# Kernel optimization log

Hardware: AMD Instinct MI355X
Metric: run time of the kernel (lower is better)

The kernel has to match this reference:

```python
import jax, jax.numpy as jnp
import numpy as np

B, N, E, A, H, F, HEADS = 2, 16384, 262144, 3, 128, 16, 4
DH = H // HEADS
CONST = (2.0 * np.pi) ** 0.5


def setup_inputs() -> dict:
    key = jax.random.key(0)
    ks = jax.random.split(key, 16)
    s = 0.05
    return {
        "x": jax.random.normal(ks[0], (B, N, H), jnp.float32),
        "edge_index": jax.random.randint(ks[1], (2, E), 0, N),
        # per-action message MLPs (self.mlp)
        "mlp_W1": jax.random.normal(ks[2], (A, H, H), jnp.float32) * s,
        "mlp_b1": jnp.zeros((A, H), jnp.float32),
        "mlp_W2": jax.random.normal(ks[3], (A, H, H), jnp.float32) * s,
        "mlp_b2": jnp.zeros((A, H), jnp.float32),
        # transformer (MMTs) projections, 4 heads over the action axis
        "Wq": jax.random.normal(ks[4], (H, H), jnp.float32) * s,
        "bq": jnp.zeros((H,), jnp.float32),
        "Wk": jax.random.normal(ks[5], (H, H), jnp.float32) * s,
        "bk": jnp.zeros((H,), jnp.float32),
        "Wv": jax.random.normal(ks[6], (H, H), jnp.float32) * s,
        "bv": jnp.zeros((H,), jnp.float32),
        "Wo": jax.random.normal(ks[7], (H, H), jnp.float32) * s,
        "bo": jnp.zeros((H,), jnp.float32),
        # decide_mu MLPs (decide_In_sigma is never used in the original forward)
        "mu_W1": jax.random.normal(ks[8], (A, H, H), jnp.float32) * s,
        "mu_b1": jnp.zeros((A, H), jnp.float32),
        "mu_W2": jax.random.normal(ks[9], (A, H, F), jnp.float32) * s,
        "mu_b2": jnp.zeros((A, F), jnp.float32),
    }


def _forward(x, edge_index, mlp_W1, mlp_b1, mlp_W2, mlp_b2,
             Wq, bq, Wk, bk, Wv, bv, Wo, bo, mu_W1, mu_b1, mu_W2, mu_b2):
    # per-action MLP stack: (B,N,H) -> (B,N,A,H)
    h = jax.nn.relu(jnp.einsum('bnh,ahk->bnak', x, mlp_W1) + mlp_b1)
    h = jnp.einsum('bnak,akh->bnah', h, mlp_W2) + mlp_b2
    # gather along source nodes, scatter-add into destination bins
    dst, src = edge_index[0], edge_index[1]
    g = h[:, src]                                   # (B,E,A,H) ~ 800 MB
    agg = jax.ops.segment_sum(jnp.moveaxis(g, 1, 0), dst, num_segments=N)
    agg = jnp.moveaxis(agg, 0, 1)                   # (B,N,A,H)
    # multi-head self-attention over the action axis (len A) per node
    q = (jnp.einsum('bnah,hk->bnak', agg, Wq) + bq).reshape(B, N, A, HEADS, DH)
    k = (jnp.einsum('bnah,hk->bnak', agg, Wk) + bk).reshape(B, N, A, HEADS, DH)
    v = (jnp.einsum('bnah,hk->bnak', agg, Wv) + bv).reshape(B, N, A, HEADS, DH)
    scores = jnp.einsum('bnqed,bnked->bneqk', q, k) / (DH ** 0.5)
    attn = jax.nn.softmax(scores, axis=-1)
    o = jnp.einsum('bneqk,bnked->bnqed', attn, v).reshape(B, N, A, H)
    h_I = agg + jnp.einsum('bnah,hk->bnak', o, Wo) + bo  # residual
    # per-action decode to action means: (B,N,A,F)
    m = jax.nn.relu(jnp.einsum('bnah,ahk->bnak', h_I, mu_W1) + mu_b1)
    mu = jnp.einsum('bnak,akf->bnaf', m, mu_W2) + mu_b2
    # Gaussian reparameterized sampling, VAR is a non-trainable all-ones buffer
    VAR = jnp.ones((N, A, F), jnp.float32)
    noise = jax.random.normal(jax.random.key(42), mu.shape, mu.dtype)
    sample = mu + noise * VAR
    logp = -jnp.log(CONST * VAR) - (sample - mu) ** 2 / (2.0 * VAR ** 2)
    a0 = jax.nn.softmax(jnp.tanh(sample[:, :, 0, :]), axis=-1)
    a1 = jax.nn.sigmoid(sample[:, :, 1, :])
    a2 = jnp.tanh(sample[:, :, 2, :])
    sample_out = jnp.stack([a0, a1, a2], axis=2)    # (B,N,A,F)
    return sample_out, logp.sum((-1, -2))           # ((B,N,A,F),(B,N))


def reference(x, edge_index, mlp_W1, mlp_b1, mlp_W2, mlp_b2,
              Wq, bq, Wk, bk, Wv, bv, Wo, bo, mu_W1, mu_b1, mu_W2, mu_b2):
    return _forward(x, edge_index, mlp_W1, mlp_b1, mlp_W2, mlp_b2,
                    Wq, bq, Wk, bk, Wv, bv, Wo, bo, mu_W1, mu_b1, mu_W2, mu_b2)
```

## Files before the change

### kernel.cpp

```cpp
#include <hip/hip_runtime.h>

#define NN    16384
#define EE    262144
#define BNODES 32768
#define AH    384
#define TOT_NOISE 1572864u

typedef __attribute__((ext_vector_type(8))) short short8;
typedef __attribute__((ext_vector_type(4))) float v4f;

__device__ __forceinline__ unsigned short f2bf(float f) {
  unsigned u = __float_as_uint(f);
  unsigned r = u + 0x7fffu + ((u >> 16) & 1u);
  return (unsigned short)(r >> 16);
}
__device__ __forceinline__ float bf2f(unsigned short h) {
  return __uint_as_float(((unsigned)h) << 16);
}
__device__ __forceinline__ float bflo(unsigned u) { return __uint_as_float(u << 16); }
__device__ __forceinline__ float bfhi(unsigned u) { return __uint_as_float(u & 0xffff0000u); }

__device__ __forceinline__ void threefry2x32_042(unsigned& x0, unsigned& x1) {
  const unsigned ks0 = 0u;
  const unsigned ks1 = 42u;
  const unsigned ks2 = 0x1BD11BDAu ^ 0u ^ 42u;
  x0 += ks0; x1 += ks1;
#define TFR(r) { x0 += x1; x1 = (x1 << (r)) | (x1 >> (32 - (r))); x1 ^= x0; }
  TFR(13) TFR(15) TFR(26) TFR(6)   x0 += ks1; x1 += ks2 + 1u;
  TFR(17) TFR(29) TFR(16) TFR(24)  x0 += ks2; x1 += ks0 + 2u;
  TFR(13) TFR(15) TFR(26) TFR(6)   x0 += ks0; x1 += ks1 + 3u;
  TFR(17) TFR(29) TFR(16) TFR(24)  x0 += ks1; x1 += ks2 + 4u;
  TFR(13) TFR(15) TFR(26) TFR(6)   x0 += ks2; x1 += ks0 + 5u;
#undef TFR
}

__device__ __forceinline__ float erfinv_f32(float x) {
  float w = -log1pf(-x * x);
  float p;
  if (w < 5.0f) {
    w -= 2.5f;
    p = 2.81022636e-08f;
    p = fmaf(p, w, 3.43273939e-07f);
    p = fmaf(p, w, -3.5233877e-06f);
    p = fmaf(p, w, -4.39150654e-06f);
    p = fmaf(p, w, 0.00021858087f);
    p = fmaf(p, w, -0.00125372503f);
    p = fmaf(p, w, -0.00417768164f);
    p = fmaf(p, w, 0.246640727f);
    p = fmaf(p, w, 1.50140941f);
  } else {
    w = sqrtf(w) - 3.0f;
    p = -0.000200214257f;
    p = fmaf(p, w, 0.000100950558f);
    p = fmaf(p, w, 0.00134934322f);
    p = fmaf(p, w, -0.00367342844f);
    p = fmaf(p, w, 0.00573950773f);
    p = fmaf(p, w, -0.0076224613f);
    p = fmaf(p, w, 0.00943887047f);
    p = fmaf(p, w, 1.00167406f);
    p = fmaf(p, w, 2.83297682f);
  }
  return p * x;
}

__device__ __forceinline__ unsigned jax_random_bits32(unsigned i) {
  unsigned x0 = 0u, x1 = i;
  threefry2x32_042(x0, x1);
  return x0 ^ x1;
}

__device__ __forceinline__ float jax_normal_from_bits(unsigned bits) {
  float f = __uint_as_float((bits >> 9) | 0x3f800000u) - 1.0f;
  const float lo = -0.99999994f;
  float u = f * 2.0f + lo;
  u = fmaxf(u, lo);
  return 1.4142135623730951f * erfinv_f32(u);
}

__global__ void edge_count(const int* __restrict__ dst, int* __restrict__ deg) {
  int e = blockIdx.x * 256 + threadIdx.x;
  if (e < EE) atomicAdd(&deg[dst[e]], 1);
}

__global__ __launch_bounds__(256) void scan_k(const int* __restrict__ deg,
                                              int* __restrict__ offs,
                                              int* __restrict__ cur) {
  __shared__ int part[256];
  int t = threadIdx.x;
  int base = t * 64;
  int s = 0;
  for (int i = 0; i < 64; i++) s += deg[base + i];
  part[t] = s;
  __syncthreads();
  for (int off = 1; off < 256; off <<= 1) {
    int v = (t >= off) ? part[t - off] : 0;
    __syncthreads();
    part[t] += v;
    __syncthreads();
  }
  int run = (t == 0) ? 0 : part[t - 1];
  for (int i = 0; i < 64; i++) {
    offs[base + i] = run;
    cur[base + i] = run;
    run += deg[base + i];
  }
  if (t == 255) offs[NN] = run;
}

__global__ void edge_fill(const int* __restrict__ dst, const int* __restrict__ srcv,
                          int* __restrict__ cur, int* __restrict__ csr) {
  int e = blockIdx.x * 256 + threadIdx.x;
  if (e < EE) {
    int d = dst[e];
    int p = atomicAdd(&cur[d], 1);
    csr[p] = srcv[e];
  }
}

__global__ __launch_bounds__(256) void prep_wfrag(
    const float* __restrict__ W1, const float* __restrict__ W2,
    const float* __restrict__ mW1,
    const float* __restrict__ Wq, const float* __restrict__ Wk,
    const float* __restrict__ Wv, const float* __restrict__ Wo,
    unsigned short* __restrict__ F) {
  int m = blockIdx.y;
  const float* W;
  if (m < 3) W = W1 + (long)m * 16384;
  else if (m < 6) W = W2 + (long)(m - 3) * 16384;
  else if (m < 9) W = mW1 + (long)(m - 6) * 16384;
  else W = (m == 9) ? Wq : (m == 10) ? Wk : (m == 11) ? Wv : Wo;
  int f = blockIdx.x * 256 + threadIdx.x;
  int tile = f >> 9;
  int kt = tile >> 3, nt = tile & 7;
  int r = f & 511;
  int lane = r >> 3, j = r & 7;
  int k = kt * 32 + (lane >> 4) * 8 + j;
  int n = nt * 16 + (lane & 15);
  F[(long)m * 16384 + f] = f2bf(W[k * 128 + n]);
}

__global__ __launch_bounds__(256) void prep_w2frag(
    const float* __restrict__ mW2, unsigned short* __restrict__ F2) {
  int a = blockIdx.y;
  int f = blockIdx.x * 256 + threadIdx.x;
  int kt = f >> 9;
  int r = f & 511;
  int lane = r >> 3, j = r & 7;
  int k = kt * 32 + (lane >> 4) * 8 + j;
  int n = lane & 15;
  F2[a * 2048 + f] = f2bf(mW2[(a * 128 + k) * 16 + n]);
}

#define GXSTR 136
__global__ __launch_bounds__(256) void gemm_bf16(
    const unsigned short* __restrict__ X, long xRowStride, long xAOff,
    const unsigned short* __restrict__ WF,
    const float* __restrict__ Bias, long bAStride,
    unsigned short* __restrict__ C, long cRowStride, long cAOff,
    int relu, int xfp32) {
  __shared__ __align__(16) unsigned short As[128 * GXSTR];
  const int a = blockIdx.y;
  const long m0 = (long)blockIdx.x * 128;
  const int tid = threadIdx.x;
  const unsigned short* Wp = WF + (long)a * 16384;

  if (xfp32) {
    const float* Xf = (const float*)X + (long)a * xAOff + m0 * xRowStride;
#pragma unroll
    for (int p = 0; p < 8; p++) {
      int c = tid + p * 256;
      int row = c >> 4, c8 = (c & 15) * 8;
      float4 v1 = *(const float4*)(Xf + (long)row * xRowStride + c8);
      float4 v2 = *(const float4*)(Xf + (long)row * xRowStride + c8 + 4);
      short8 o;
      o[0] = (short)f2bf(v1.x); o[1] = (short)f2bf(v1.y);
      o[2] = (short)f2bf(v1.z); o[3] = (short)f2bf(v1.w);
      o[4] = (short)f2bf(v2.x); o[5] = (short)f2bf(v2.y);
      o[6] = (short)f2bf(v2.z); o[7] = (short)f2bf(v2.w);
      *(short8*)(&As[row * GXSTR + c8]) = o;
    }
  } else {
    const unsigned short* Xp = X + (long)a * xAOff + m0 * xRowStride;
#pragma unroll
    for (int p = 0; p < 8; p++) {
      int c = tid + p * 256;
      int row = c >> 4, c8 = (c & 15) * 8;
      short8 v = *(const short8*)(Xp + (long)row * xRowStride + c8);
      *(short8*)(&As[row * GXSTR + c8]) = v;
    }
  }
  __syncthreads();

  const int w = tid >> 6;
  const int l = tid & 63;
  const int lr = l & 15;
  const int lg = l >> 4;

  v4f acc[8][2];
#pragma unroll
  for (int mt = 0; mt < 8; mt++) {
    acc[mt][0] = (v4f){0.f, 0.f, 0.f, 0.f};
    acc[mt][1] = (v4f){0.f, 0.f, 0.f, 0.f};
  }

#pragma unroll
  for (int kt = 0; kt < 4; kt++) {
    short8 bfr[2];
#pragma unroll
    for (int ntl = 0; ntl < 2; ntl++)
      bfr[ntl] = *(const short8*)(Wp + (long)(kt * 8 + 2 * w + ntl) * 512 + l * 8);
#pragma unroll
    for (int mt = 0; mt < 8; mt++) {
      short8 af = *(const short8*)(&As[(mt * 16 + lr) * GXSTR + kt * 32 + lg * 8]);
      acc[mt][0] = __builtin_amdgcn_mfma_f32_16x16x32_bf16(af, bfr[0], acc[mt][0], 0, 0, 0);
      acc[mt][1] = __builtin_amdgcn_mfma_f32_16x16x32_bf16(af, bfr[1], acc[mt][1], 0, 0, 0);
    }
  }

  float bv[2] = {Bias[(long)a * bAStride + 32 * w + lr],
                 Bias[(long)a * bAStride + 32 * w + 16 + lr]};
#pragma unroll
  for (int mt = 0; mt < 8; mt++)
#pragma unroll
    for (int ntl = 0; ntl < 2; ntl++)
#pragma unroll
      for (int i = 0; i < 4; i++) {
        long row = m0 + mt * 16 + lg * 4 + i;
        int col = 32 * w + ntl * 16 + lr;
        float t = acc[mt][ntl][i] + bv[ntl];
        if (relu) t = fmaxf(t, 0.0f);
        C[row * cRowStride + (long)a * cAOff + col] = f2bf(t);
      }
}

__global__ __launch_bounds__(192) void aggregate_bf2(
    const unsigned short* __restrict__ H, const int* __restrict__ offs,
    const int* __restrict__ csr, unsigned short* __restrict__ AGB) {
  const int n = blockIdx.x;
  const int t = threadIdx.x;
  const int bt = t / 96;
  const int c = (t % 96) * 4;
  const int e0 = offs[n], e1 = offs[n + 1];
  const unsigned short* hb = H + (long)bt * NN * 384 + c;
  float a0 = 0.f, a1 = 0.f, a2 = 0.f, a3 = 0.f;
  int j = e0;
  for (; j + 4 <= e1; j += 4) {
    int s0 = csr[j], s1 = csr[j + 1], s2 = csr[j + 2], s3 = csr[j + 3];
    uint2 u0 = *(const uint2*)(hb + (long)s0 * 384);
    uint2 u1 = *(const uint2*)(hb + (long)s1 * 384);
    uint2 u2 = *(const uint2*)(hb + (long)s2 * 384);
    uint2 u3 = *(const uint2*)(hb + (long)s3 * 384);
    a0 += bflo(u0.x); a1 += bfhi(u0.x); a2 += bflo(u0.y); a3 += bfhi(u0.y);
    a0 += bflo(u1.x); a1 += bfhi(u1.x); a2 += bflo(u1.y); a3 += bfhi(u1.y);
    a0 += bflo(u2.x); a1 += bfhi(u2.x); a2 += bflo(u2.y); a3 += bfhi(u2.y);
    a0 += bflo(u3.x); a1 += bfhi(u3.x); a2 += bflo(u3.y); a3 += bfhi(u3.y);
  }
  for (; j < e1; j++) {
    int s = csr[j];
    uint2 u = *(const uint2*)(hb + (long)s * 384);
    a0 += bflo(u.x); a1 += bfhi(u.x); a2 += bflo(u.y); a3 += bfhi(u.y);
  }
  uint2 out;
  out.x = (unsigned)f2bf(a0) | ((unsigned)f2bf(a1) << 16);
  out.y = (unsigned)f2bf(a2) | ((unsigned)f2bf(a3) << 16);
  *(uint2*)(AGB + ((long)bt * NN + n) * 384 + c) = out;
}

#define XSTR 136
#define QSTR 34
__global__ __launch_bounds__(256, 3) void attn_mfma(
    const unsigned short* __restrict__ AGB, const unsigned short* __restrict__ WF,
    const float* __restrict__ bq, const float* __restrict__ bk,
    const float* __restrict__ bv, const float* __restrict__ bo,
    unsigned short* __restrict__ OUTB) {
  __shared__ __align__(16) unsigned short xS[48 * XSTR];
  __shared__ __align__(16) unsigned short qS[4 * 48 * QSTR];
  __shared__ __align__(16) unsigned short kS[4 * 48 * QSTR];
  __shared__ __align__(16) unsigned short vS[4 * 48 * QSTR];

  const int tid = threadIdx.x;
  const long node0 = (long)blockIdx.x * 16;
  const unsigned short* src = AGB + node0 * 384;

#pragma unroll
  for (int p = 0; p < 3; p++) {
    int c = tid + p * 256;
    int row = c >> 4, c8 = (c & 15) * 8;
    short8 v = *(const short8*)(src + c * 8);
    *(short8*)(&xS[row * XSTR + c8]) = v;
  }
  __syncthreads();

  const int w = tid >> 6;
  const int l = tid & 63;
  const int lr = l & 15;
  const int lg = l >> 4;
  const unsigned short* WQ = WF;
  const unsigned short* WK = WF + 16384;
  const unsigned short* WV = WF + 32768;
  const unsigned short* WO = WF + 49152;

  v4f accq[3][2], acck[3][2], accv[3][2];
#pragma unroll
  for (int mt = 0; mt < 3; mt++)
#pragma unroll
    for (int n = 0; n < 2; n++) {
      accq[mt][n] = (v4f){0.f, 0.f, 0.f, 0.f};
      acck[mt][n] = (v4f){0.f, 0.f, 0.f, 0.f};
      accv[mt][n] = (v4f){0.f, 0.f, 0.f, 0.f};
    }

#pragma unroll
  for (int kt = 0; kt < 4; kt++) {
    short8 af[3];
#pragma unroll
    for (int mt = 0; mt < 3; mt++)
      af[mt] = *(const short8*)&xS[(mt * 16 + lr) * XSTR + kt * 32 + lg * 8];
#pragma unroll
    for (int ntl = 0; ntl < 2; ntl++) {
      long tf = (long)(kt * 8 + 2 * w + ntl) * 512 + l * 8;
      short8 b0 = *(const short8*)&WQ[tf];
      short8 b1 = *(const short8*)&WK[tf];
      short8 b2 = *(const short8*)&WV[tf];
#pragma unroll
      for (int mt = 0; mt < 3; mt++) {
        accq[mt][ntl] = __builtin_amdgcn_mfma_f32_16x16x32_bf16(af[mt], b0, accq[mt][ntl], 0, 0, 0);
        acck[mt][ntl] = __builtin_amdgcn_mfma_f32_16x16x32_bf16(af[mt], b1, acck[mt][ntl], 0, 0, 0);
        accv[mt][ntl] = __builtin_amdgcn_mfma_f32_16x16x32_bf16(af[mt], b2, accv[mt][ntl], 0, 0, 0);
      }
    }
  }

  {
    const float scale = 0.17677669529663687f;
    unsigned short* qw = &qS[w * 48 * QSTR];
    unsigned short* kw = &kS[w * 48 * QSTR];
    unsigned short* vw = &vS[w * 48 * QSTR];
    float bqv[2] = {bq[32 * w + lr], bq[32 * w + 16 + lr]};
    float bkv[2] = {bk[32 * w + lr], bk[32 * w + 16 + lr]};
    float bvv[2] = {bv[32 * w + lr], bv[32 * w + 16 + lr]};
#pragma unroll
    for (int mt = 0; mt < 3; mt++)
#pragma unroll
      for (int ntl = 0; ntl < 2; ntl++)
#pragma unroll
        for (int i = 0; i < 4; i++) {
          int row = mt * 16 + lg * 4 + i;
          int col = ntl * 16 + lr;
          qw[row * QSTR + col] = f2bf((accq[mt][ntl][i] + bqv[ntl]) * scale);
          kw[row * QSTR + col] = f2bf(acck[mt][ntl][i] + bkv[ntl]);
          vw[row * QSTR + col] = f2bf(accv[mt][ntl][i] + bvv[ntl]);
        }
  }

  float resv[3][2][4];
#pragma unroll
  for (int mt = 0; mt < 3; mt++)
#pragma unroll
    for (int ntl = 0; ntl < 2; ntl++)
#pragma unroll
      for (int i = 0; i < 4; i++)
        resv[mt][ntl][i] =
            bf2f(xS[(mt * 16 + lg * 4 + i) * XSTR + 32 * w + ntl * 16 + lr]);
  __syncthreads();

  if (l < 48) {
    int aq = l % 3;
    int ndr = l - aq;
    const unsigned* qr = (const unsigned*)&qS[(w * 48 + l) * QSTR];
    const unsigned* kr0 = (const unsigned*)&kS[(w * 48 + ndr) * QSTR];
    const unsigned* kr1 = (const unsigned*)&kS[(w * 48 + ndr + 1) * QSTR];
    const unsigned* kr2 = (const unsigned*)&kS[(w * 48 + ndr + 2) * QSTR];
    float s0 = 0.f, s1 = 0.f, s2 = 0.f;
#pragma unroll
    for (int j = 0; j < 16; j++) {
      unsigned uq = qr[j], u0 = kr0[j], u1 = kr1[j], u2 = kr2[j];
      float qa = bflo(uq), qb = bfhi(uq);
      s0 = fmaf(qa, bflo(u0), fmaf(qb, bfhi(u0), s0));
      s1 = fmaf(qa, bflo(u1), fmaf(qb, bfhi(u1), s1));
      s2 = fmaf(qa, bflo(u2), fmaf(qb, bfhi(u2), s2));
    }
    float mx = fmaxf(s0, fmaxf(s1, s2));
    float e0 = expf(s0 - mx), e1 = expf(s1 - mx), e2 = expf(s2 - mx);
    float inv = 1.0f / (e0 + e1 + e2);
    e0 *= inv; e1 *= inv; e2 *= inv;
    const unsigned* vr0 = (const unsigned*)&vS[(w * 48 + ndr) * QSTR];
    const unsigned* vr1 = (const unsigned*)&vS[(w * 48 + ndr + 1) * QSTR];
    const unsigned* vr2 = (const unsigned*)&vS[(w * 48 + ndr + 2) * QSTR];
    unsigned ov[16];
#pragma unroll
    for (int j = 0; j < 16; j++) {
      unsigned u0 = vr0[j], u1 = vr1[j], u2 = vr2[j];
      float oa = fmaf(e0, bflo(u0), fmaf(e1, bflo(u1), e2 * bflo(u2)));
      float ob = fmaf(e0, bfhi(u0), fmaf(e1, bfhi(u1), e2 * bfhi(u2)));
      ov[j] = (unsigned)f2bf(oa) | ((unsigned)f2bf(ob) << 16);
    }
    uint4* orow = (uint4*)&xS[l * XSTR + 32 * w];
    orow[0] = make_uint4(ov[0], ov[1], ov[2], ov[3]);
    orow[1] = make_uint4(ov[4], ov[5], ov[6], ov[7]);
    orow[2] = make_uint4(ov[8], ov[9], ov[10], ov[11]);
    orow[3] = make_uint4(ov[12], ov[13], ov[14], ov[15]);
  }
  __syncthreads();

  v4f acco[3][2];
#pragma unroll
  for (int mt = 0; mt < 3; mt++)
#pragma unroll
    for (int n = 0; n < 2; n++) acco[mt][n] = (v4f){0.f, 0.f, 0.f, 0.f};

#pragma unroll
  for (int kt = 0; kt < 4; kt++) {
    short8 af[3];
#pragma unroll
    for (int mt = 0; mt < 3; mt++)
      af[mt] = *(const short8*)&xS[(mt * 16 + lr) * XSTR + kt * 32 + lg * 8];
#pragma unroll
    for (int ntl = 0; ntl < 2; ntl++) {
      long tf = (long)(kt * 8 + 2 * w + ntl) * 512 + l * 8;
      short8 b = *(const short8*)&WO[tf];
#pragma unroll
      for (int mt = 0; mt < 3; mt++)
        acco[mt][ntl] = __builtin_amdgcn_mfma_f32_16x16x32_bf16(af[mt], b, acco[mt][ntl], 0, 0, 0);
    }
  }

  {
    float bov[2] = {bo[32 * w + lr], bo[32 * w + 16 + lr]};
#pragma unroll
    for (int mt = 0; mt < 3; mt++)
#pragma unroll
      for (int ntl = 0; ntl < 2; ntl++)
#pragma unroll
        for (int i = 0; i < 4; i++) {
          int row = mt * 16 + lg * 4 + i;
          int gcol = 32 * w + ntl * 16 + lr;
          OUTB[(node0 * 3 + row) * 128 + gcol] =
              f2bf(acco[mt][ntl][i] + bov[ntl] + resv[mt][ntl][i]);
        }
  }
}

#define MSTR 136
__global__ __launch_bounds__(256) void mu_final(
    const unsigned short* __restrict__ M, const unsigned short* __restrict__ WF2,
    const float* __restrict__ mb2,
    float* __restrict__ out0, float* __restrict__ out1) {
  __shared__ __align__(16) unsigned short As[192 * MSTR];
  __shared__ float lpS[192];
  const int tid = threadIdx.x;
  const long bn0 = (long)blockIdx.x * 64;

#pragma unroll
  for (int p = 0; p < 12; p++) {
    int ch = tid + p * 256;
    int nd = ch / 48;
    int rest = ch % 48;
    int a = rest >> 4;
    int k8 = (rest & 15) * 8;
    short8 v = *(const short8*)(M + (bn0 + nd) * 384 + a * 128 + k8);
    *(short8*)(&As[(a * 64 + nd) * MSTR + k8]) = v;
  }
  __syncthreads();

  const int w = tid >> 6, l = tid & 63, lr = l & 15, lg = l >> 4;

  v4f acc[3];
#pragma unroll
  for (int t = 0; t < 3; t++) acc[t] = (v4f){0.f, 0.f, 0.f, 0.f};

#pragma unroll
  for (int kt = 0; kt < 4; kt++) {
#pragma unroll
    for (int t = 0; t < 3; t++) {
      int tile = 3 * w + t;
      int a = tile >> 2;
      short8 af = *(const short8*)(&As[(tile * 16 + lr) * MSTR + kt * 32 + lg * 8]);
      short8 bf = *(const short8*)(WF2 + a * 2048 + kt * 512 + l * 8);
      acc[t] = __builtin_amdgcn_mfma_f32_16x16x32_bf16(af, bf, acc[t], 0, 0, 0);
    }
  }

#pragma unroll
  for (int t = 0; t < 3; t++) {
    int tile = 3 * w + t;
    int a = tile >> 2;
    int ndbase = (tile & 3) * 16;
    float bias = mb2[a * 16 + lr];
#pragma unroll
    for (int i = 0; i < 4; i++) {
      int nd = ndbase + lg * 4 + i;
      float mu = acc[t][i] + bias;
      unsigned gidx = (unsigned)((bn0 + nd) * 48 + a * 16 + lr);
      unsigned bits = jax_random_bits32(gidx);
      float noise = jax_normal_from_bits(bits);
      float sample = mu + noise;
      float lp = -0.9189385332046727f - 0.5f * noise * noise;
      lp += __shfl_xor(lp, 1, 64);
      lp += __shfl_xor(lp, 2, 64);
      lp += __shfl_xor(lp, 4, 64);
      lp += __shfl_xor(lp, 8, 64);
      if (lr == 0) lpS[a * 64 + nd] = lp;
      float res;
      if (a == 0) {
        float th = tanhf(sample);
        float mx = th;
        mx = fmaxf(mx, __shfl_xor(mx, 1, 64));
        mx = fmaxf(mx, __shfl_xor(mx, 2, 64));
        mx = fmaxf(mx, __shfl_xor(mx, 4, 64));
        mx = fmaxf(mx, __shfl_xor(mx, 8, 64));
        float ex = expf(th - mx);
        float ss = ex;
        ss += __shfl_xor(ss, 1, 64);
        ss += __shfl_xor(ss, 2, 64);
        ss += __shfl_xor(ss, 4, 64);
        ss += __shfl_xor(ss, 8, 64);
        res = ex / ss;
      } else if (a == 1) {
        res = 1.0f / (1.0f + expf(-sample));
      } else {
        res = tanhf(sample);
      }
      out0[gidx] = res;
    }
  }
  __syncthreads();
  if (tid < 64)
    out1[bn0 + tid] = lpS[tid] + lpS[64 + tid] + lpS[128 + tid];
}

extern "C" void kernel_launch(void* const* d_in, const int* in_sizes, int n_in,
                              void* d_out, int out_size, void* d_ws, size_t ws_size,
                              hipStream_t stream) {
  const float* x = (const float*)d_in[0];
  const int* ei = (const int*)d_in[1];
  const float* W1 = (const float*)d_in[2];
  const float* b1 = (const float*)d_in[3];
  const float* W2 = (const float*)d_in[4];
  const float* b2 = (const float*)d_in[5];
  const float* Wq = (const float*)d_in[6];
  const float* bq = (const float*)d_in[7];
  const float* Wk = (const float*)d_in[8];
  const float* bk = (const float*)d_in[9];
  const float* Wv = (const float*)d_in[10];
  const float* bv = (const float*)d_in[11];
  const float* Wo = (const float*)d_in[12];
  const float* bo = (const float*)d_in[13];
  const float* mW1 = (const float*)d_in[14];
  const float* mb1 = (const float*)d_in[15];
  const float* mW2 = (const float*)d_in[16];
  const float* mb2 = (const float*)d_in[17];
  (void)in_sizes; (void)n_in; (void)out_size; (void)ws_size;

  unsigned short* T1 = (unsigned short*)d_ws;
  unsigned short* HB = T1 + 12582912;
  unsigned short* AGB = HB + 12582912;
  int* deg = (int*)(AGB + 12582912);
  int* offs = deg + NN;
  int* cur = offs + (NN + 1);
  int* csr = cur + NN;
  unsigned short* wfrag = (unsigned short*)(((uintptr_t)(csr + EE) + 15) & ~(uintptr_t)15);
  unsigned short* w2frag = wfrag + 13 * 16384;

  const int* dst = ei;
  const int* srcv = ei + EE;

  float* out0 = (float*)d_out;
  float* out1 = out0 + TOT_NOISE;

  hipMemsetAsync(deg, 0, NN * sizeof(int), stream);
  edge_count<<<EE / 256, 256, 0, stream>>>(dst, deg);
  scan_k<<<1, 256, 0, stream>>>(deg, offs, cur);
  edge_fill<<<EE / 256, 256, 0, stream>>>(dst, srcv, cur, csr);
  prep_wfrag<<<dim3(64, 13), 256, 0, stream>>>(W1, W2, mW1, Wq, Wk, Wv, Wo, wfrag);
  prep_w2frag<<<dim3(8, 3), 256, 0, stream>>>(mW2, w2frag);

  dim3 g128(BNODES / 128, 3);
  gemm_bf16<<<g128, 256, 0, stream>>>((const unsigned short*)x, 128, 0, wfrag, b1, 128, T1, AH, 128, 1, 1);
  gemm_bf16<<<g128, 256, 0, stream>>>(T1, AH, 128, wfrag + 3 * 16384, b2, 128, HB, AH, 128, 0, 0);
  aggregate_bf2<<<NN, 192, 0, stream>>>(HB, offs, csr, AGB);
  attn_mfma<<<BNODES / 16, 256, 0, stream>>>(AGB, wfrag + 9 * 16384, bq, bk, bv, bo, T1);
  gemm_bf16<<<g128, 256, 0, stream>>>(T1, AH, 128, wfrag + 6 * 16384, mb1, 128, HB, AH, 128, 1, 0);
  mu_final<<<BNODES / 64, 256, 0, stream>>>(HB, w2frag, mb2, out0, out1);
}
```

Measured before the change: 277.3 us.

## Fuse MLP GEMMs, merge decode into attention, restructure aggregation with prefetch

The two per-action MLP GEMMs become one kernel that keeps the intermediate activation in shared memory instead of writing and rereading it from global memory. The mu decode MLP and the sampling epilogue move into the attention kernel, so the attention output no longer round-trips through global memory and two launches disappear. The aggregation kernel now maps each block to two nodes of one batch and prefetches CSR indices in groups of eight. The attention kernel becomes longer and heavier on registers, and the aggregation now reads each CSR range once per batch instead of sharing it across both batches in one block.

```diff
diff --git a/kernel.cpp b/kernel.cpp
--- a/kernel.cpp
+++ b/kernel.cpp
@@ -152,49 +152,34 @@
 }
 
 #define GXSTR 136
-__global__ __launch_bounds__(256) void gemm_bf16(
-    const unsigned short* __restrict__ X, long xRowStride, long xAOff,
-    const unsigned short* __restrict__ WF,
-    const float* __restrict__ Bias, long bAStride,
-    unsigned short* __restrict__ C, long cRowStride, long cAOff,
-    int relu, int xfp32) {
+__global__ __launch_bounds__(256, 4) void mlp_fused(
+    const float* __restrict__ X,
+    const unsigned short* __restrict__ WF1, const float* __restrict__ b1,
+    const unsigned short* __restrict__ WF2, const float* __restrict__ b2,
+    unsigned short* __restrict__ H) {
   __shared__ __align__(16) unsigned short As[128 * GXSTR];
   const int a = blockIdx.y;
   const long m0 = (long)blockIdx.x * 128;
   const int tid = threadIdx.x;
-  const unsigned short* Wp = WF + (long)a * 16384;
-
-  if (xfp32) {
-    const float* Xf = (const float*)X + (long)a * xAOff + m0 * xRowStride;
-#pragma unroll
-    for (int p = 0; p < 8; p++) {
-      int c = tid + p * 256;
-      int row = c >> 4, c8 = (c & 15) * 8;
-      float4 v1 = *(const float4*)(Xf + (long)row * xRowStride + c8);
-      float4 v2 = *(const float4*)(Xf + (long)row * xRowStride + c8 + 4);
-      short8 o;
-      o[0] = (short)f2bf(v1.x); o[1] = (short)f2bf(v1.y);
-      o[2] = (short)f2bf(v1.z); o[3] = (short)f2bf(v1.w);
-      o[4] = (short)f2bf(v2.x); o[5] = (short)f2bf(v2.y);
-      o[6] = (short)f2bf(v2.z); o[7] = (short)f2bf(v2.w);
-      *(short8*)(&As[row * GXSTR + c8]) = o;
-    }
-  } else {
-    const unsigned short* Xp = X + (long)a * xAOff + m0 * xRowStride;
-#pragma unroll
-    for (int p = 0; p < 8; p++) {
-      int c = tid + p * 256;
-      int row = c >> 4, c8 = (c & 15) * 8;
-      short8 v = *(const short8*)(Xp + (long)row * xRowStride + c8);
-      *(short8*)(&As[row * GXSTR + c8]) = v;
-    }
-  }
-  __syncthreads();
-
-  const int w = tid >> 6;
-  const int l = tid & 63;
-  const int lr = l & 15;
-  const int lg = l >> 4;
+  const unsigned short* Wp1 = WF1 + (long)a * 16384;
+  const unsigned short* Wp2 = WF2 + (long)a * 16384;
+
+#pragma unroll
+  for (int p = 0; p < 8; p++) {
+    int c = tid + p * 256;
+    int row = c >> 4, c8 = (c & 15) * 8;
+    float4 v1 = *(const float4*)(X + (m0 + row) * 128 + c8);
+    float4 v2 = *(const float4*)(X + (m0 + row) * 128 + c8 + 4);
+    short8 o;
+    o[0] = (short)f2bf(v1.x); o[1] = (short)f2bf(v1.y);
+    o[2] = (short)f2bf(v1.z); o[3] = (short)f2bf(v1.w);
+    o[4] = (short)f2bf(v2.x); o[5] = (short)f2bf(v2.y);
+    o[6] = (short)f2bf(v2.z); o[7] = (short)f2bf(v2.w);
+    *(short8*)(&As[row * GXSTR + c8]) = o;
+  }
+  __syncthreads();
+
+  const int w = tid >> 6, l = tid & 63, lr = l & 15, lg = l >> 4;
 
   v4f acc[8][2];
 #pragma unroll
@@ -202,13 +187,12 @@
     acc[mt][0] = (v4f){0.f, 0.f, 0.f, 0.f};
     acc[mt][1] = (v4f){0.f, 0.f, 0.f, 0.f};
   }
-
 #pragma unroll
   for (int kt = 0; kt < 4; kt++) {
     short8 bfr[2];
 #pragma unroll
     for (int ntl = 0; ntl < 2; ntl++)
-      bfr[ntl] = *(const short8*)(Wp + (long)(kt * 8 + 2 * w + ntl) * 512 + l * 8);
+      bfr[ntl] = *(const short8*)(Wp1 + (long)(kt * 8 + 2 * w + ntl) * 512 + l * 8);
 #pragma unroll
     for (int mt = 0; mt < 8; mt++) {
       short8 af = *(const short8*)(&As[(mt * 16 + lr) * GXSTR + kt * 32 + lg * 8]);
@@ -216,48 +200,93 @@
       acc[mt][1] = __builtin_amdgcn_mfma_f32_16x16x32_bf16(af, bfr[1], acc[mt][1], 0, 0, 0);
     }
   }
-
-  float bv[2] = {Bias[(long)a * bAStride + 32 * w + lr],
-                 Bias[(long)a * bAStride + 32 * w + 16 + lr]};
-#pragma unroll
-  for (int mt = 0; mt < 8; mt++)
+  __syncthreads();
+
+  {
+    float bv[2] = {b1[a * 128 + 32 * w + lr], b1[a * 128 + 32 * w + 16 + lr]};
+#pragma unroll
+    for (int mt = 0; mt < 8; mt++)
+#pragma unroll
+      for (int ntl = 0; ntl < 2; ntl++)
+#pragma unroll
+        for (int i = 0; i < 4; i++) {
+          int row = mt * 16 + lg * 4 + i;
+          int col = 32 * w + ntl * 16 + lr;
+          As[row * GXSTR + col] = f2bf(fmaxf(acc[mt][ntl][i] + bv[ntl], 0.0f));
+        }
+  }
+  __syncthreads();
+
+#pragma unroll
+  for (int mt = 0; mt < 8; mt++) {
+    acc[mt][0] = (v4f){0.f, 0.f, 0.f, 0.f};
+    acc[mt][1] = (v4f){0.f, 0.f, 0.f, 0.f};
+  }
+#pragma unroll
+  for (int kt = 0; kt < 4; kt++) {
+    short8 bfr[2];
 #pragma unroll
     for (int ntl = 0; ntl < 2; ntl++)
-#pragma unroll
-      for (int i = 0; i < 4; i++) {
-        long row = m0 + mt * 16 + lg * 4 + i;
-        int col = 32 * w + ntl * 16 + lr;
-        float t = acc[mt][ntl][i] + bv[ntl];
-        if (relu) t = fmaxf(t, 0.0f);
-        C[row * cRowStride + (long)a * cAOff + col] = f2bf(t);
-      }
-}
-
-__global__ __launch_bounds__(192) void aggregate_bf2(
+      bfr[ntl] = *(const short8*)(Wp2 + (long)(kt * 8 + 2 * w + ntl) * 512 + l * 8);
+#pragma unroll
+    for (int mt = 0; mt < 8; mt++) {
+      short8 af = *(const short8*)(&As[(mt * 16 + lr) * GXSTR + kt * 32 + lg * 8]);
+      acc[mt][0] = __builtin_amdgcn_mfma_f32_16x16x32_bf16(af, bfr[0], acc[mt][0], 0, 0, 0);
+      acc[mt][1] = __builtin_amdgcn_mfma_f32_16x16x32_bf16(af, bfr[1], acc[mt][1], 0, 0, 0);
+    }
+  }
+  {
+    float bv[2] = {b2[a * 128 + 32 * w + lr], b2[a * 128 + 32 * w + 16 + lr]};
+#pragma unroll
+    for (int mt = 0; mt < 8; mt++)
+#pragma unroll
+      for (int ntl = 0; ntl < 2; ntl++)
+#pragma unroll
+        for (int i = 0; i < 4; i++) {
+          long row = m0 + mt * 16 + lg * 4 + i;
+          int col = 32 * w + ntl * 16 + lr;
+          H[row * 384 + a * 128 + col] = f2bf(acc[mt][ntl][i] + bv[ntl]);
+        }
+  }
+}
+
+__global__ __launch_bounds__(192) void aggregate_v3(
     const unsigned short* __restrict__ H, const int* __restrict__ offs,
     const int* __restrict__ csr, unsigned short* __restrict__ AGB) {
-  const int n = blockIdx.x;
+  const int bid = blockIdx.x;
+  const int bt = bid >> 13;
+  const int pair = bid & 8191;
   const int t = threadIdx.x;
-  const int bt = t / 96;
+  const int n = pair * 2 + (t / 96);
   const int c = (t % 96) * 4;
   const int e0 = offs[n], e1 = offs[n + 1];
   const unsigned short* hb = H + (long)bt * NN * 384 + c;
   float a0 = 0.f, a1 = 0.f, a2 = 0.f, a3 = 0.f;
-  int j = e0;
-  for (; j + 4 <= e1; j += 4) {
-    int s0 = csr[j], s1 = csr[j + 1], s2 = csr[j + 2], s3 = csr[j + 3];
-    uint2 u0 = *(const uint2*)(hb + (long)s0 * 384);
-    uint2 u1 = *(const uint2*)(hb + (long)s1 * 384);
-    uint2 u2 = *(const uint2*)(hb + (long)s2 * 384);
-    uint2 u3 = *(const uint2*)(hb + (long)s3 * 384);
-    a0 += bflo(u0.x); a1 += bfhi(u0.x); a2 += bflo(u0.y); a3 += bfhi(u0.y);
-    a0 += bflo(u1.x); a1 += bfhi(u1.x); a2 += bflo(u1.y); a3 += bfhi(u1.y);
-    a0 += bflo(u2.x); a1 += bfhi(u2.x); a2 += bflo(u2.y); a3 += bfhi(u2.y);
-    a0 += bflo(u3.x); a1 += bfhi(u3.x); a2 += bflo(u3.y); a3 += bfhi(u3.y);
-  }
-  for (; j < e1; j++) {
-    int s = csr[j];
-    uint2 u = *(const uint2*)(hb + (long)s * 384);
+
+  const int nfull = (e1 - e0) >> 3;
+  int s[8];
+  if (nfull > 0) {
+#pragma unroll
+    for (int i = 0; i < 8; i++) s[i] = csr[e0 + i];
+  }
+  for (int b = 0; b < nfull; b++) {
+    int sn[8];
+    if (b + 1 < nfull) {
+      int base = e0 + b * 8 + 8;
+#pragma unroll
+      for (int i = 0; i < 8; i++) sn[i] = csr[base + i];
+    }
+#pragma unroll
+    for (int i = 0; i < 8; i++) {
+      uint2 u = *(const uint2*)(hb + (long)s[i] * 384);
+      a0 += bflo(u.x); a1 += bfhi(u.x); a2 += bflo(u.y); a3 += bfhi(u.y);
+    }
+#pragma unroll
+    for (int i = 0; i < 8; i++) s[i] = sn[i];
+  }
+  for (int j = e0 + nfull * 8; j < e1; j++) {
+    int si = csr[j];
+    uint2 u = *(const uint2*)(hb + (long)si * 384);
     a0 += bflo(u.x); a1 += bfhi(u.x); a2 += bflo(u.y); a3 += bfhi(u.y);
   }
   uint2 out;
@@ -268,15 +297,18 @@
 
 #define XSTR 136
 #define QSTR 34
-__global__ __launch_bounds__(256, 3) void attn_mfma(
+__global__ __launch_bounds__(256, 3) void attn_mega(
     const unsigned short* __restrict__ AGB, const unsigned short* __restrict__ WF,
     const float* __restrict__ bq, const float* __restrict__ bk,
     const float* __restrict__ bv, const float* __restrict__ bo,
-    unsigned short* __restrict__ OUTB) {
+    const unsigned short* __restrict__ WM1, const float* __restrict__ mb1,
+    const unsigned short* __restrict__ WM2, const float* __restrict__ mb2,
+    float* __restrict__ out0, float* __restrict__ out1) {
   __shared__ __align__(16) unsigned short xS[48 * XSTR];
   __shared__ __align__(16) unsigned short qS[4 * 48 * QSTR];
   __shared__ __align__(16) unsigned short kS[4 * 48 * QSTR];
   __shared__ __align__(16) unsigned short vS[4 * 48 * QSTR];
+  __shared__ float lpS[48];
 
   const int tid = threadIdx.x;
   const long node0 = (long)blockIdx.x * 16;
@@ -309,7 +341,6 @@
       acck[mt][n] = (v4f){0.f, 0.f, 0.f, 0.f};
       accv[mt][n] = (v4f){0.f, 0.f, 0.f, 0.f};
     }
-
 #pragma unroll
   for (int kt = 0; kt < 4; kt++) {
     short8 af[3];
@@ -330,7 +361,6 @@
       }
     }
   }
-
   {
     const float scale = 0.17677669529663687f;
     unsigned short* qw = &qS[w * 48 * QSTR];
@@ -408,7 +438,6 @@
   for (int mt = 0; mt < 3; mt++)
 #pragma unroll
     for (int n = 0; n < 2; n++) acco[mt][n] = (v4f){0.f, 0.f, 0.f, 0.f};
-
 #pragma unroll
   for (int kt = 0; kt < 4; kt++) {
     short8 af[3];
@@ -424,6 +453,7 @@
         acco[mt][ntl] = __builtin_amdgcn_mfma_f32_16x16x32_bf16(af[mt], b, acco[mt][ntl], 0, 0, 0);
     }
   }
+  __syncthreads();
 
   {
     float bov[2] = {bo[32 * w + lr], bo[32 * w + 16 + lr]};
@@ -434,64 +464,62 @@
 #pragma unroll
         for (int i = 0; i < 4; i++) {
           int row = mt * 16 + lg * 4 + i;
+          int nd = row / 3, a_ = row - nd * 3;
           int gcol = 32 * w + ntl * 16 + lr;
-          OUTB[(node0 * 3 + row) * 128 + gcol] =
+          xS[(a_ * 16 + nd) * XSTR + gcol] =
               f2bf(acco[mt][ntl][i] + bov[ntl] + resv[mt][ntl][i]);
         }
   }
-}
-
-#define MSTR 136
-__global__ __launch_bounds__(256) void mu_final(
-    const unsigned short* __restrict__ M, const unsigned short* __restrict__ WF2,
-    const float* __restrict__ mb2,
-    float* __restrict__ out0, float* __restrict__ out1) {
-  __shared__ __align__(16) unsigned short As[192 * MSTR];
-  __shared__ float lpS[192];
-  const int tid = threadIdx.x;
-  const long bn0 = (long)blockIdx.x * 64;
-
-#pragma unroll
-  for (int p = 0; p < 12; p++) {
-    int ch = tid + p * 256;
-    int nd = ch / 48;
-    int rest = ch % 48;
-    int a = rest >> 4;
-    int k8 = (rest & 15) * 8;
-    short8 v = *(const short8*)(M + (bn0 + nd) * 384 + a * 128 + k8);
-    *(short8*)(&As[(a * 64 + nd) * MSTR + k8]) = v;
-  }
-  __syncthreads();
-
-  const int w = tid >> 6, l = tid & 63, lr = l & 15, lg = l >> 4;
-
-  v4f acc[3];
-#pragma unroll
-  for (int t = 0; t < 3; t++) acc[t] = (v4f){0.f, 0.f, 0.f, 0.f};
-
+  __syncthreads();
+
+  v4f accm[3][2];
+#pragma unroll
+  for (int mt = 0; mt < 3; mt++)
+#pragma unroll
+    for (int n = 0; n < 2; n++) accm[mt][n] = (v4f){0.f, 0.f, 0.f, 0.f};
 #pragma unroll
   for (int kt = 0; kt < 4; kt++) {
 #pragma unroll
-    for (int t = 0; t < 3; t++) {
-      int tile = 3 * w + t;
-      int a = tile >> 2;
-      short8 af = *(const short8*)(&As[(tile * 16 + lr) * MSTR + kt * 32 + lg * 8]);
-      short8 bf = *(const short8*)(WF2 + a * 2048 + kt * 512 + l * 8);
-      acc[t] = __builtin_amdgcn_mfma_f32_16x16x32_bf16(af, bf, acc[t], 0, 0, 0);
-    }
-  }
-
-#pragma unroll
-  for (int t = 0; t < 3; t++) {
-    int tile = 3 * w + t;
-    int a = tile >> 2;
-    int ndbase = (tile & 3) * 16;
-    float bias = mb2[a * 16 + lr];
+    for (int mt = 0; mt < 3; mt++) {
+      short8 af = *(const short8*)&xS[(mt * 16 + lr) * XSTR + kt * 32 + lg * 8];
+#pragma unroll
+      for (int ntl = 0; ntl < 2; ntl++) {
+        short8 b = *(const short8*)(WM1 + (long)mt * 16384 +
+                                    (long)(kt * 8 + 2 * w + ntl) * 512 + l * 8);
+        accm[mt][ntl] = __builtin_amdgcn_mfma_f32_16x16x32_bf16(af, b, accm[mt][ntl], 0, 0, 0);
+      }
+    }
+  }
+  __syncthreads();
+
+#pragma unroll
+  for (int mt = 0; mt < 3; mt++)
+#pragma unroll
+    for (int ntl = 0; ntl < 2; ntl++) {
+      int col = 32 * w + ntl * 16 + lr;
+      float bias = mb1[mt * 128 + col];
+#pragma unroll
+      for (int i = 0; i < 4; i++) {
+        int rowp = mt * 16 + lg * 4 + i;
+        xS[rowp * XSTR + col] = f2bf(fmaxf(accm[mt][ntl][i] + bias, 0.0f));
+      }
+    }
+  __syncthreads();
+
+  if (w < 3) {
+    v4f accu = (v4f){0.f, 0.f, 0.f, 0.f};
+#pragma unroll
+    for (int kt = 0; kt < 4; kt++) {
+      short8 af = *(const short8*)&xS[(w * 16 + lr) * XSTR + kt * 32 + lg * 8];
+      short8 b = *(const short8*)(WM2 + w * 2048 + kt * 512 + l * 8);
+      accu = __builtin_amdgcn_mfma_f32_16x16x32_bf16(af, b, accu, 0, 0, 0);
+    }
+    float bias = mb2[w * 16 + lr];
 #pragma unroll
     for (int i = 0; i < 4; i++) {
-      int nd = ndbase + lg * 4 + i;
-      float mu = acc[t][i] + bias;
-      unsigned gidx = (unsigned)((bn0 + nd) * 48 + a * 16 + lr);
+      int nd = lg * 4 + i;
+      float mu = accu[i] + bias;
+      unsigned gidx = (unsigned)((node0 + nd) * 48 + w * 16 + lr);
       unsigned bits = jax_random_bits32(gidx);
       float noise = jax_normal_from_bits(bits);
       float sample = mu + noise;
@@ -500,9 +528,9 @@
       lp += __shfl_xor(lp, 2, 64);
       lp += __shfl_xor(lp, 4, 64);
       lp += __shfl_xor(lp, 8, 64);
-      if (lr == 0) lpS[a * 64 + nd] = lp;
+      if (lr == 0) lpS[w * 16 + nd] = lp;
       float res;
-      if (a == 0) {
+      if (w == 0) {
         float th = tanhf(sample);
         float mx = th;
         mx = fmaxf(mx, __shfl_xor(mx, 1, 64));
@@ -516,7 +544,7 @@
         ss += __shfl_xor(ss, 4, 64);
         ss += __shfl_xor(ss, 8, 64);
         res = ex / ss;
-      } else if (a == 1) {
+      } else if (w == 1) {
         res = 1.0f / (1.0f + expf(-sample));
       } else {
         res = tanhf(sample);
@@ -525,8 +553,8 @@
     }
   }
   __syncthreads();
-  if (tid < 64)
-    out1[bn0 + tid] = lpS[tid] + lpS[64 + tid] + lpS[128 + tid];
+  if (tid < 16)
+    out1[node0 + tid] = lpS[tid] + lpS[16 + tid] + lpS[32 + tid];
 }
 
 extern "C" void kernel_launch(void* const* d_in, const int* in_sizes, int n_in,
@@ -552,8 +580,7 @@
   const float* mb2 = (const float*)d_in[17];
   (void)in_sizes; (void)n_in; (void)out_size; (void)ws_size;
 
-  unsigned short* T1 = (unsigned short*)d_ws;
-  unsigned short* HB = T1 + 12582912;
+  unsigned short* HB = (unsigned short*)d_ws;
   unsigned short* AGB = HB + 12582912;
   int* deg = (int*)(AGB + 12582912);
   int* offs = deg + NN;
@@ -575,11 +602,9 @@
   prep_wfrag<<<dim3(64, 13), 256, 0, stream>>>(W1, W2, mW1, Wq, Wk, Wv, Wo, wfrag);
   prep_w2frag<<<dim3(8, 3), 256, 0, stream>>>(mW2, w2frag);
 
-  dim3 g128(BNODES / 128, 3);
-  gemm_bf16<<<g128, 256, 0, stream>>>((const unsigned short*)x, 128, 0, wfrag, b1, 128, T1, AH, 128, 1, 1);
-  gemm_bf16<<<g128, 256, 0, stream>>>(T1, AH, 128, wfrag + 3 * 16384, b2, 128, HB, AH, 128, 0, 0);
-  aggregate_bf2<<<NN, 192, 0, stream>>>(HB, offs, csr, AGB);
-  attn_mfma<<<BNODES / 16, 256, 0, stream>>>(AGB, wfrag + 9 * 16384, bq, bk, bv, bo, T1);
-  gemm_bf16<<<g128, 256, 0, stream>>>(T1, AH, 128, wfrag + 6 * 16384, mb1, 128, HB, AH, 128, 1, 0);
-  mu_final<<<BNODES / 64, 256, 0, stream>>>(HB, w2frag, mb2, out0, out1);
-}
+  mlp_fused<<<dim3(BNODES / 128, 3), 256, 0, stream>>>(x, wfrag, b1, wfrag + 3 * 16384, b2, HB);
+  aggregate_v3<<<2 * NN / 2, 192, 0, stream>>>(HB, offs, csr, AGB);
+  attn_mega<<<BNODES / 16, 256, 0, stream>>>(AGB, wfrag + 9 * 16384, bq, bk, bv, bo,
+                                             wfrag + 6 * 16384, mb1, w2frag, mb2,
+                                             out0, out1);
+}
```

Result: faster. 250.1 us (-9.8%).
